# Performance work log

Measured on AMD Instinct MI355X. Metric: run time of the kernel, lower is better.

## Reference

```python
import jax, jax.numpy as jnp
import numpy as np

# Config (matches init_kwargs + Mamba2 defaults: expand=2, headdim=64, ngroups=1)
B_, C_IN, T, H, W = 4, 23, 8, 128, 128
P = 4
DM = 256
D_STATE = 16
D_CONV = 4
EXPAND = 2
D_INNER = EXPAND * DM            # 512
HEADDIM = 64
NHEADS = D_INNER // HEADDIM      # 8
CONV_DIM = D_INNER + 2 * D_STATE # 544 (ngroups=1)
D_IN_PROJ = 2 * D_INNER + 2 * D_STATE + NHEADS


def setup_inputs() -> dict:
    key = jax.random.key(0)
    ks = jax.random.split(key, 12)
    s = lambda k, shape, sc: (jax.random.normal(k, shape, jnp.float32) * sc)
    x = jax.random.normal(ks[0], (B_, C_IN, T, H, W), jnp.float32)
    patch_w = s(ks[1], (DM, C_IN, P, P), 0.05)       # Conv3d weight, depth-1 dim squeezed
    patch_b = s(ks[2], (DM,), 0.02)
    W_in = s(ks[3], (DM, D_IN_PROJ), 0.05)           # in_proj (bias=False)
    conv_w = s(ks[4], (CONV_DIM, D_CONV), 0.2)       # depthwise conv1d weight
    conv_b = s(ks[5], (CONV_DIM,), 0.02)
    dt_bias = jnp.log(jnp.expm1(jnp.exp(jax.random.uniform(ks[6], (NHEADS,), jnp.float32, jnp.log(1e-3), jnp.log(1e-1)))))
    A_log = jnp.log(jnp.arange(1, NHEADS + 1, dtype=jnp.float32))
    D_param = jnp.ones((NHEADS,), jnp.float32)
    norm_w = jnp.ones((D_INNER,), jnp.float32)
    W_out = s(ks[7], (D_INNER, DM), 0.05)            # out_proj (bias=False)
    unembed_w = s(ks[8], (DM, C_IN, P, P), 0.05)     # ConvTranspose3d weight (in,out,1,p,p)
    unembed_b = s(ks[9], (C_IN,), 0.02)
    return {"x": x, "patch_w": patch_w, "patch_b": patch_b, "W_in": W_in,
            "conv_w": conv_w, "conv_b": conv_b, "dt_bias": dt_bias, "A_log": A_log,
            "D_param": D_param, "norm_w": norm_w, "W_out": W_out,
            "unembed_w": unembed_w, "unembed_b": unembed_b}


def reference(x, patch_w, patch_b, W_in, conv_w, conv_b, dt_bias, A_log,
              D_param, norm_w, W_out, unembed_w, unembed_b):
    B, C, Tt, Hh, Ww = x.shape
    p = patch_w.shape[-1]
    Hp, Wp = Hh // p, Ww // p
    L = Tt * Hp * Wp
    # --- Conv3d patch embed (kernel (1,p,p), stride (1,p,p)) == non-overlapping patchify ---
    xr = x.reshape(B, C, Tt, Hp, p, Wp, p)
    emb = jnp.einsum('bcthiwj,dcij->bthwd', xr, patch_w) + patch_b  # [B,T,Hp,Wp,D]
    xs = emb.reshape(B, L, DM)
    # --- Mamba2 ---
    zxbcdt = xs @ W_in                                 # [B,L,2*d_inner+2*d_state+nheads]
    z = zxbcdt[:, :, :D_INNER]
    xBC = zxbcdt[:, :, D_INNER:D_INNER + CONV_DIM]
    dt = zxbcdt[:, :, D_INNER + CONV_DIM:]             # [B,L,nheads]
    # causal depthwise conv1d + silu
    xp = jnp.pad(xBC, ((0, 0), (D_CONV - 1, 0), (0, 0)))
    conv_out = conv_b + sum(xp[:, k:k + L, :] * conv_w[:, k] for k in range(D_CONV))
    xBC = jax.nn.silu(conv_out)
    xh = xBC[:, :, :D_INNER].reshape(B, L, NHEADS, HEADDIM)
    Bm = xBC[:, :, D_INNER:D_INNER + D_STATE]          # [B,L,N] (ngroups=1)
    Cm = xBC[:, :, D_INNER + D_STATE:]                 # [B,L,N]
    dt = jax.nn.softplus(dt + dt_bias)                 # [B,L,H]
    A = -jnp.exp(A_log)                                # [H]
    dA = jnp.exp(dt * A)                               # [B,L,H]
    xdt = xh * dt[..., None]                           # [B,L,H,P]
    # selective state-space scan: h_t = dA_t h_{t-1} + (dt_t x_t) B_t^T ; y_t = h_t C_t
    def step(h, inp):
        dA_t, xdt_t, B_t, C_t = inp
        h = dA_t[..., None, None] * h + jnp.einsum('bhp,bn->bhpn', xdt_t, B_t)
        y = jnp.einsum('bhpn,bn->bhp', h, C_t)
        return h, y
    inps = (dA.transpose(1, 0, 2), xdt.transpose(1, 0, 2, 3),
            Bm.transpose(1, 0, 2), Cm.transpose(1, 0, 2))
    h0 = jnp.zeros((B, NHEADS, HEADDIM, D_STATE), xs.dtype)
    _, ys = jax.lax.scan(step, h0, inps)               # [L,B,H,P]
    y = ys.transpose(1, 0, 2, 3) + D_param[None, None, :, None] * xh
    y = y.reshape(B, L, D_INNER)
    # gated RMSNorm (norm_before_gate=False): rmsnorm(y * silu(z)) * w
    yg = y * jax.nn.silu(z)
    y = yg * jax.lax.rsqrt(jnp.mean(yg * yg, axis=-1, keepdims=True) + 1e-5) * norm_w
    out_seq = y @ W_out                                # [B,L,DM]
    # --- ConvTranspose3d unembed (kernel (1,p,p), stride (1,p,p)) == un-patchify ---
    outp = out_seq.reshape(B, Tt, Hp, Wp, DM)
    un = jnp.einsum('bthwd,dcij->bcthiwj', outp, unembed_w)
    out = un.reshape(B, C, Tt, Hh, Ww) + unembed_b[None, :, None, None, None]
    return out + x
```

## Files before the change

kernel.cpp:

```cpp
#include <hip/hip_runtime.h>
#include <hip/hip_bf16.h>
#include <cstdint>
#include <cstddef>

#define B_N       4
#define C_INCH    23
#define T_N       8
#define W_IMG     128
#define L_SEQ     8192
#define BLROWS    32768
#define DM_       256
#define D_INNER_  512
#define CONV_DIM_ 544
#define D_PROJ    1064
#define KPATCH    368
#define QCH       64
#define NCH       128
#define RECW      56
#define PFD       8

typedef unsigned short ushort_t;
typedef unsigned int uint_t;
typedef __attribute__((ext_vector_type(8))) short short8;
typedef __attribute__((ext_vector_type(4))) float f32x4;

__device__ __forceinline__ float b2f(ushort_t u) {
    union { float f; uint_t u; } v; v.u = ((uint_t)u) << 16; return v.f;
}
__device__ __forceinline__ ushort_t f2b(float f) {
    union { float f; uint_t u; } v; v.f = f;
    uint_t r = v.u + 0x7fffu + ((v.u >> 16) & 1u);
    return (ushort_t)(r >> 16);
}

__device__ __forceinline__ void gload_lds16(const ushort_t* g, ushort_t* l) {
    __builtin_amdgcn_global_load_lds(
        (const __attribute__((address_space(1))) unsigned int*)g,
        (__attribute__((address_space(3))) unsigned int*)l, 16, 0, 0);
}

__device__ __forceinline__ short8 frag8(const float* q, bool live) {
    short8 f;
    if (live) {
        float4 lo = *(const float4*)q, hi = *(const float4*)(q + 4);
        f[0] = (short)f2b(lo.x); f[1] = (short)f2b(lo.y);
        f[2] = (short)f2b(lo.z); f[3] = (short)f2b(lo.w);
        f[4] = (short)f2b(hi.x); f[5] = (short)f2b(hi.y);
        f[6] = (short)f2b(hi.z); f[7] = (short)f2b(hi.w);
    } else {
        #pragma unroll
        for (int e = 0; e < 8; ++e) f[e] = 0;
    }
    return f;
}

__global__ void k_transcast(const float* __restrict__ src, ushort_t* __restrict__ dst,
                            int K, int N, const float* __restrict__ rscale) {
    int n = blockIdx.x;
    for (int k = threadIdx.x; k < K; k += 256) {
        float v = 0.f;
        if (n < N) {
            v = src[(size_t)k * N + n];
            if (rscale) v *= rscale[k];
        }
        dst[(size_t)n * K + k] = f2b(v);
    }
}

__global__ void k_castpad(const float* __restrict__ src, ushort_t* __restrict__ dst) {
    int d = blockIdx.x; int k = threadIdx.x;
    dst[d * 384 + k] = (k < KPATCH) ? f2b(src[d * KPATCH + k]) : (ushort_t)0;
}

__global__ void __launch_bounds__(256) k_pgemm(const float* __restrict__ x,
                                               const ushort_t* __restrict__ Wt,
                                               ushort_t* __restrict__ Cv,
                                               const float* __restrict__ bias) {
    __shared__ ushort_t Al[128 * 64];
    __shared__ ushort_t Bl[128 * 64];
    const int tid = threadIdx.x;
    const int w = tid >> 6, lane = tid & 63;
    const int wr = w >> 1, wc = w & 1;
    const int rowbase = blockIdx.y * 128;
    const int colbase = blockIdx.x * 128;
    const int g = lane >> 4, r = lane & 15;
    const int b  = rowbase >> 13;
    const int t  = (rowbase >> 10) & 7;
    const int hp0 = (rowbase >> 5) & 31;

    f32x4 acc[4][4];
    #pragma unroll
    for (int i = 0; i < 4; ++i)
        #pragma unroll
        for (int j = 0; j < 4; ++j) acc[i][j] = (f32x4){0.f, 0.f, 0.f, 0.f};

    for (int it = 0; it < 6; ++it) {
        int k0 = it * 64;
        __syncthreads();
        #pragma unroll
        for (int i2 = 0; i2 < 4; ++i2) {
            int s = i2 * 256 + (w << 6) + lane;
            int row = s >> 3;
            int c16 = (s & 7) ^ (row & 7);
            gload_lds16(Wt + (size_t)(colbase + row) * 384 + k0 + c16 * 8,
                        &Bl[(size_t)(i2 * 256 + (w << 6)) * 8]);
        }
        #pragma unroll
        for (int i2 = 0; i2 < 8; ++i2) {
            int idx = i2 * 256 + tid;
            int row = idx >> 4, kq = idx & 15;
            int c = (k0 >> 4) + (kq >> 2);
            int i = kq & 3;
            uint_t u0 = 0, u1 = 0;
            if (c < C_INCH) {
                int hp = hp0 + (row >> 5), wp = row & 31;
                const float4 v = *(const float4*)&x[(((size_t)(b * C_INCH + c) * T_N + t) << 14)
                                                    + (size_t)(hp * 4 + i) * W_IMG + wp * 4];
                u0 = (uint_t)f2b(v.x) | ((uint_t)f2b(v.y) << 16);
                u1 = (uint_t)f2b(v.z) | ((uint_t)f2b(v.w) << 16);
            }
            int slot = (row << 3) + ((kq >> 1) ^ (row & 7));
            *(uint2*)&Al[(size_t)slot * 8 + (kq & 1) * 4] = make_uint2(u0, u1);
        }
        __syncthreads();

        short8 af[2][4], bf[2][4];
        #pragma unroll
        for (int ks = 0; ks < 2; ++ks)
            #pragma unroll
            for (int mi = 0; mi < 4; ++mi) {
                int row = (wr << 6) + (mi << 4) + r;
                int c16 = ((ks << 2) | g) ^ (row & 7);
                af[ks][mi] = *(const short8*)&Al[(size_t)((row << 3) + c16) * 8];
            }
        #pragma unroll
        for (int ks = 0; ks < 2; ++ks)
            #pragma unroll
            for (int ni = 0; ni < 4; ++ni) {
                int row = (wc << 6) + (ni << 4) + r;
                int c16 = ((ks << 2) | g) ^ (row & 7);
                bf[ks][ni] = *(const short8*)&Bl[(size_t)((row << 3) + c16) * 8];
            }
        #pragma unroll
        for (int ks = 0; ks < 2; ++ks)
            #pragma unroll
            for (int mi = 0; mi < 4; ++mi)
                #pragma unroll
                for (int ni = 0; ni < 4; ++ni)
                    acc[mi][ni] = __builtin_amdgcn_mfma_f32_16x16x32_bf16(
                        af[ks][mi], bf[ks][ni], acc[mi][ni], 0, 0, 0);
    }

    #pragma unroll
    for (int mi = 0; mi < 4; ++mi) {
        int rw = rowbase + (wr << 6) + (mi << 4) + (g << 2);
        #pragma unroll
        for (int ni = 0; ni < 4; ++ni) {
            int col = colbase + (wc << 6) + (ni << 4) + r;
            float bv = bias[col];
            f32x4 v = acc[mi][ni];
            #pragma unroll
            for (int j = 0; j < 4; ++j)
                Cv[(size_t)(rw + j) * DM_ + col] = f2b(v[j] + bv);
        }
    }
}

template <int K, int N, bool CBF, bool ASCALE>
__global__ void __launch_bounds__(256) k_mgemm(const ushort_t* __restrict__ A, const int lda,
                                               const ushort_t* __restrict__ Wt,
                                               void* __restrict__ Cv, const int ldc, const int coff,
                                               const float* __restrict__ bias) {
    __shared__ ushort_t Al[128 * 64];
    __shared__ ushort_t Bl[128 * 64];
    const int tid = threadIdx.x;
    const int w = tid >> 6, lane = tid & 63;
    const int wr = w >> 1, wc = w & 1;
    const int rowbase = blockIdx.y * 128;
    const int colbase = blockIdx.x * 128;
    const int g = lane >> 4, r = lane & 15;

    f32x4 acc[4][4];
    #pragma unroll
    for (int i = 0; i < 4; ++i)
        #pragma unroll
        for (int j = 0; j < 4; ++j) acc[i][j] = (f32x4){0.f, 0.f, 0.f, 0.f};
    float rs[4] = {0.f, 0.f, 0.f, 0.f};

    for (int k0 = 0; k0 < K; k0 += 64) {
        __syncthreads();
        #pragma unroll
        for (int it = 0; it < 4; ++it) {
            int s = it * 256 + (w << 6) + lane;
            int row = s >> 3;
            int c16 = (s & 7) ^ (row & 7);
            gload_lds16(A + (size_t)(rowbase + row) * lda + k0 + c16 * 8,
                        &Al[(size_t)(it * 256 + (w << 6)) * 8]);
        }
        #pragma unroll
        for (int it = 0; it < 4; ++it) {
            int s = it * 256 + (w << 6) + lane;
            int row = s >> 3;
            int c16 = (s & 7) ^ (row & 7);
            gload_lds16(Wt + (size_t)(colbase + row) * K + k0 + c16 * 8,
                        &Bl[(size_t)(it * 256 + (w << 6)) * 8]);
        }
        __syncthreads();

        short8 af[2][4], bf[2][4];
        #pragma unroll
        for (int ks = 0; ks < 2; ++ks)
            #pragma unroll
            for (int mi = 0; mi < 4; ++mi) {
                int row = (wr << 6) + (mi << 4) + r;
                int c16 = ((ks << 2) | g) ^ (row & 7);
                af[ks][mi] = *(const short8*)&Al[(size_t)((row << 3) + c16) * 8];
            }
        #pragma unroll
        for (int ks = 0; ks < 2; ++ks)
            #pragma unroll
            for (int ni = 0; ni < 4; ++ni) {
                int row = (wc << 6) + (ni << 4) + r;
                int c16 = ((ks << 2) | g) ^ (row & 7);
                bf[ks][ni] = *(const short8*)&Bl[(size_t)((row << 3) + c16) * 8];
            }
        if (ASCALE) {
            #pragma unroll
            for (int ks = 0; ks < 2; ++ks)
                #pragma unroll
                for (int mi = 0; mi < 4; ++mi)
                    #pragma unroll
                    for (int e = 0; e < 8; ++e) {
                        float v = b2f((ushort_t)af[ks][mi][e]);
                        rs[mi] += v * v;
                    }
        }
        #pragma unroll
        for (int ks = 0; ks < 2; ++ks)
            #pragma unroll
            for (int mi = 0; mi < 4; ++mi)
                #pragma unroll
                for (int ni = 0; ni < 4; ++ni)
                    acc[mi][ni] = __builtin_amdgcn_mfma_f32_16x16x32_bf16(
                        af[ks][mi], bf[ks][ni], acc[mi][ni], 0, 0, 0);
    }

    #pragma unroll
    for (int mi = 0; mi < 4; ++mi) {
        int rw = rowbase + (wr << 6) + (mi << 4) + (g << 2);
        float sj[4] = {1.f, 1.f, 1.f, 1.f};
        if (ASCALE) {
            float s = rs[mi];
            s += __shfl_xor(s, 16);
            s += __shfl_xor(s, 32);
            float sc = rsqrtf(s * (1.f / 512.f) + 1e-5f);
            #pragma unroll
            for (int j = 0; j < 4; ++j) sj[j] = __shfl(sc, 4 * g + j);
        }
        #pragma unroll
        for (int ni = 0; ni < 4; ++ni) {
            int col = colbase + (wc << 6) + (ni << 4) + r;
            if (col < N) {
                float bv = bias ? bias[col] : 0.f;
                f32x4 v = acc[mi][ni];
                #pragma unroll
                for (int j = 0; j < 4; ++j) {
                    size_t cidx = (size_t)(rw + j) * ldc + coff + col;
                    float vr = v[j] * sj[j] + bv;
                    if (CBF) ((ushort_t*)Cv)[cidx] = f2b(vr);
                    else     ((float*)Cv)[cidx]   = vr;
                }
            }
        }
    }
}

__global__ void __launch_bounds__(256) k_conv(const ushort_t* __restrict__ xbcdt,
                                              const float* __restrict__ cw,
                                              const float* __restrict__ cb,
                                              const float* __restrict__ dtb,
                                              const float* __restrict__ alog,
                                              ushort_t* __restrict__ xbc,
                                              float* __restrict__ brec) {
    int tid = threadIdx.x;
    int rb = blockIdx.x * 8;
    int srb = rb & (L_SEQ - 1);
    #pragma unroll
    for (int it = 0; it < 3; ++it) {
        int ch = it * 256 + tid;
        if (ch >= 552) break;
        if (ch < CONV_DIM_) {
            float w0 = cw[ch * 4 + 0], w1 = cw[ch * 4 + 1];
            float w2 = cw[ch * 4 + 2], w3 = cw[ch * 4 + 3];
            float bias = cb[ch];
            float win[11];
            #pragma unroll
            for (int j = 0; j < 11; ++j) {
                int sj = srb + j - 3;
                win[j] = (sj >= 0) ? b2f(xbcdt[(size_t)(rb + j - 3) * 640 + ch]) : 0.f;
            }
            #pragma unroll
            for (int r = 0; r < 8; ++r) {
                float acc = bias + win[r] * w0 + win[r + 1] * w1 + win[r + 2] * w2 + win[r + 3] * w3;
                float s = acc / (1.f + __expf(-acc));
                size_t row = rb + r;
                if (ch < 512) xbc[row * 512 + ch] = f2b(s);
                else          brec[row * RECW + (ch - 512)] = s;
            }
        } else {
            int h = ch - CONV_DIM_;
            float A = -__expf(alog[h]);
            float db = dtb[h];
            #pragma unroll
            for (int r = 0; r < 8; ++r) {
                size_t row = rb + r;
                float v = b2f(xbcdt[row * 640 + ch]) + db;
                float sp = (v > 20.f) ? v : log1pf(__expf(v));
                brec[row * RECW + 32 + h] = __expf(sp * A);
                brec[row * RECW + 40 + h] = sp;
                brec[row * RECW + 48 + h] = sp * A;
            }
        }
    }
}

__global__ void __launch_bounds__(256) k_scan1(const ushort_t* __restrict__ xbc,
                                               const float* __restrict__ brec,
                                               float* __restrict__ sbuf,
                                               float* __restrict__ cdf) {
    __shared__ float rec[QCH * RECW];
    int c = blockIdx.x, b = blockIdx.z;
    int tid = threadIdx.x;
    int h = blockIdx.y * 4 + (tid >> 6);
    int p = tid & 63;
    int off = h * 64 + p;
    size_t row0 = (size_t)b * L_SEQ + (size_t)c * QCH;

    {
        const float4* src = (const float4*)(brec + row0 * RECW);
        float4* dst = (float4*)rec;
        #pragma unroll
        for (int i = 0; i < 3; ++i) dst[i * 256 + tid] = src[i * 256 + tid];
        if (tid < 128) dst[768 + tid] = src[768 + tid];
    }

    float st[16];
    #pragma unroll
    for (int n = 0; n < 16; ++n) st[n] = 0.f;
    float cd = 1.f;
    float xh[PFD];
    #pragma unroll
    for (int j = 0; j < PFD; ++j) xh[j] = b2f(xbc[(row0 + j) * 512 + off]);
    __syncthreads();

    for (int s0 = 0; s0 < QCH; s0 += PFD) {
        float xhn[PFD];
        #pragma unroll
        for (int j = 0; j < PFD; ++j)
            xhn[j] = b2f(xbc[(row0 + s0 + PFD + j) * 512 + off]);
        #pragma unroll
        for (int j = 0; j < PFD; ++j) {
            const float* r = rec + (s0 + j) * RECW;
            float da  = r[32 + h];
            float dtt = r[40 + h];
            float xdt = xh[j] * dtt;
            const float4* B4 = (const float4*)r;
            #pragma unroll
            for (int q = 0; q < 4; ++q) {
                float4 Bv = B4[q];
                st[q*4+0] = da * st[q*4+0] + xdt * Bv.x;
                st[q*4+1] = da * st[q*4+1] + xdt * Bv.y;
                st[q*4+2] = da * st[q*4+2] + xdt * Bv.z;
                st[q*4+3] = da * st[q*4+3] + xdt * Bv.w;
            }
            cd *= da;
        }
        #pragma unroll
        for (int j = 0; j < PFD; ++j) xh[j] = xhn[j];
    }
    size_t base = (size_t)((b * 8 + h) * NCH + c) * 1024 + p * 16;
    #pragma unroll
    for (int q = 0; q < 4; ++q)
        *(float4*)&sbuf[base + q * 4] = make_float4(st[q*4], st[q*4+1], st[q*4+2], st[q*4+3]);
    if (p == 0) cdf[(b * 8 + h) * NCH + c] = cd;
}

__global__ void __launch_bounds__(256) k_chain(const float* __restrict__ sbuf,
                                               const float* __restrict__ cdf,
                                               float* __restrict__ hin) {
    int h = blockIdx.x, b = blockIdx.y;
    int tid = threadIdx.x;
    float4 H = make_float4(0.f, 0.f, 0.f, 0.f);
    size_t base = (size_t)((b * 8 + h) * NCH) * 1024;
    for (int c = 0; c < NCH; ++c) {
        *(float4*)&hin[base + (size_t)c * 1024 + tid * 4] = H;
        float cdfv = cdf[(b * 8 + h) * NCH + c];
        float4 S = *(const float4*)&sbuf[base + (size_t)c * 1024 + tid * 4];
        H.x = cdfv * H.x + S.x;
        H.y = cdfv * H.y + S.y;
        H.z = cdfv * H.z + S.z;
        H.w = cdfv * H.w + S.w;
    }
}

__global__ void __launch_bounds__(64) k_ssc2(const ushort_t* __restrict__ xbc,
                                             const ushort_t* __restrict__ z_bf,
                                             const float* __restrict__ brec,
                                             const float* __restrict__ Dp,
                                             const float* __restrict__ hin,
                                             ushort_t* __restrict__ yg_out) {
    __shared__ ushort_t XhT[64 * 72];
    __shared__ ushort_t Pl [64 * 72];
    __shared__ float Sl[64], Tl[64], El[64];
    const int c = blockIdx.x, h = blockIdx.y, b = blockIdx.z;
    const int lane = threadIdx.x;
    const int g = lane >> 4, r = lane & 15;
    const size_t row0 = (size_t)b * L_SEQ + (size_t)c * QCH;
    const size_t bhc = (size_t)(b * 8 + h) * NCH + c;

    uint4 xw[8];
    {
        const uint4* xsrc = (const uint4*)(xbc + (row0 + lane) * 512 + h * 64);
        #pragma unroll
        for (int q = 0; q < 8; ++q) xw[q] = xsrc[q];
    }
    float ldA = brec[(row0 + lane) * RECW + 48 + h];
    float dtv = brec[(row0 + lane) * RECW + 40 + h];

    float S = ldA;
    #pragma unroll
    for (int d = 1; d < 64; d <<= 1) {
        float o = __shfl(S, (lane >= d) ? (lane - d) : 0);
        if (lane >= d) S += o;
    }
    Sl[lane] = S;
    Tl[lane] = S - __logf(dtv);
    El[lane] = __expf(S);

    #pragma unroll
    for (int p = 0; p < 64; ++p) {
        uint4 v = xw[p >> 3];
        int sub = (p >> 1) & 3;
        uint_t word = (sub == 0) ? v.x : (sub == 1) ? v.y : (sub == 2) ? v.z : v.w;
        XhT[p * 72 + lane] = (ushort_t)((p & 1) ? (word >> 16) : (word & 0xffffu));
    }

    short8 cwf[4], bwf[4];
    #pragma unroll
    for (int t4 = 0; t4 < 4; ++t4) {
        cwf[t4] = frag8(brec + (row0 + t4 * 16 + r) * RECW + 16 + g * 8, g < 2);
        bwf[t4] = frag8(brec + (row0 + t4 * 16 + r) * RECW + 0  + g * 8, g < 2);
    }
    __syncthreads();

    #pragma unroll
    for (int j0t = 0; j0t < 4; ++j0t) {
        #pragma unroll
        for (int i0t = 0; i0t < 4; ++i0t) {
            f32x4 m = (f32x4){0.f, 0.f, 0.f, 0.f};
            m = __builtin_amdgcn_mfma_f32_16x16x32_bf16(bwf[j0t], cwf[i0t], m, 0, 0, 0);
            int i = i0t * 16 + r;
            float si = Sl[i];
            float4 tj = *(const float4*)&Tl[j0t * 16 + g * 4];
            ushort_t pv[4];
            #pragma unroll
            for (int reg = 0; reg < 4; ++reg) {
                int j = j0t * 16 + g * 4 + reg;
                float tjv = (reg == 0) ? tj.x : (reg == 1) ? tj.y : (reg == 2) ? tj.z : tj.w;
                float mask = (j <= i) ? __expf(si - tjv) : 0.f;
                pv[reg] = f2b(m[reg] * mask);
            }
            uint2 packed = make_uint2((uint_t)pv[0] | ((uint_t)pv[1] << 16),
                                      (uint_t)pv[2] | ((uint_t)pv[3] << 16));
            *(uint2*)&Pl[i * 72 + j0t * 16 + g * 4] = packed;
        }
    }
    __syncthreads();

    short8 xhf[4][2];
    #pragma unroll
    for (int p0t = 0; p0t < 4; ++p0t)
        #pragma unroll
        for (int kk = 0; kk < 2; ++kk)
            xhf[p0t][kk] = *(const short8*)&XhT[(p0t * 16 + r) * 72 + kk * 32 + g * 8];
    short8 hinf[4];
    #pragma unroll
    for (int p0t = 0; p0t < 4; ++p0t)
        hinf[p0t] = frag8(hin + bhc * 1024 + (size_t)(p0t * 16 + r) * 16 + g * 8, g < 2);

    const float Dh = Dp[h];

    #pragma unroll
    for (int i0t = 0; i0t < 4; ++i0t) {
        short8 pa0 = *(const short8*)&Pl[(i0t * 16 + r) * 72 + 0  + g * 8];
        short8 pa1 = *(const short8*)&Pl[(i0t * 16 + r) * 72 + 32 + g * 8];
        float4 e4 = *(const float4*)&El[i0t * 16 + g * 4];
        #pragma unroll
        for (int p0t = 0; p0t < 4; ++p0t) {
            f32x4 acc = (f32x4){0.f, 0.f, 0.f, 0.f};
            acc = __builtin_amdgcn_mfma_f32_16x16x32_bf16(cwf[i0t], hinf[p0t], acc, 0, 0, 0);
            acc[0] *= e4.x; acc[1] *= e4.y; acc[2] *= e4.z; acc[3] *= e4.w;
            acc = __builtin_amdgcn_mfma_f32_16x16x32_bf16(pa0, xhf[p0t][0], acc, 0, 0, 0);
            acc = __builtin_amdgcn_mfma_f32_16x16x32_bf16(pa1, xhf[p0t][1], acc, 0, 0, 0);
            int p = p0t * 16 + r;
            #pragma unroll
            for (int reg = 0; reg < 4; ++reg) {
                int i = i0t * 16 + g * 4 + reg;
                size_t row = row0 + i;
                float xhv = b2f(XhT[p * 72 + i]);
                float y = acc[reg] + Dh * xhv;
                float zz = b2f(z_bf[row * 512 + h * 64 + p]);
                float ygv = y * (zz / (1.f + __expf(-zz)));
                yg_out[row * 512 + h * 64 + p] = f2b(ygv);
            }
        }
    }
}

__global__ void __launch_bounds__(256) k_scatter(const ushort_t* __restrict__ tmp,
                                                 const float* __restrict__ ub,
                                                 const float* __restrict__ xin,
                                                 float* __restrict__ out) {
    int tid = threadIdx.x;
    int w = tid & 127;
    int h = (blockIdx.x << 1) | (tid >> 7);
    int c = blockIdx.y >> 3, t = blockIdx.y & 7;
    int b = blockIdx.z;
    size_t row = (size_t)b * L_SEQ + t * 1024 + (h >> 2) * 32 + (w >> 2);
    int kk = c * 16 + (h & 3) * 4 + (w & 3);
    size_t oidx = (((size_t)(b * C_INCH + c) * T_N + t) << 14) + (size_t)h * W_IMG + w;
    out[oidx] = b2f(tmp[row * KPATCH + kk]) + ub[c] + xin[oidx];
}

extern "C" void kernel_launch(void* const* d_in, const int* in_sizes, int n_in,
                              void* d_out, int out_size, void* d_ws, size_t ws_size,
                              hipStream_t stream) {
    const float* x       = (const float*)d_in[0];
    const float* patch_w = (const float*)d_in[1];
    const float* patch_b = (const float*)d_in[2];
    const float* W_in    = (const float*)d_in[3];
    const float* conv_w  = (const float*)d_in[4];
    const float* conv_b  = (const float*)d_in[5];
    const float* dt_bias = (const float*)d_in[6];
    const float* A_log   = (const float*)d_in[7];
    const float* D_param = (const float*)d_in[8];
    const float* norm_w  = (const float*)d_in[9];
    const float* W_out   = (const float*)d_in[10];
    const float* unemb_w = (const float*)d_in[11];
    const float* unemb_b = (const float*)d_in[12];
    float* out = (float*)d_out;

    char* p = (char*)d_ws;
    ushort_t* scratch = (ushort_t*)p; p += (size_t)BLROWS * 384 * 2;
    float* cdf  = (float*)p;   p += (size_t)32 * NCH * 4;
    float* sbuf = (float*)p;   p += (size_t)32 * NCH * 1024 * 4;
    float* hin  = (float*)p;   p += (size_t)32 * NCH * 1024 * 4;
    float* brec = (float*)p;   p += (size_t)BLROWS * RECW * 4;
    ushort_t* Wt_p   = (ushort_t*)p; p += (size_t)256 * 384 * 2;
    ushort_t* Wt_in  = (ushort_t*)p; p += (size_t)1152 * 256 * 2;
    ushort_t* Wt_out = (ushort_t*)p; p += (size_t)256 * 512 * 2;
    ushort_t* Wt_un  = (ushort_t*)p; p += (size_t)384 * 256 * 2;
    ushort_t* xs     = (ushort_t*)p; p += (size_t)BLROWS * DM_ * 2;
    ushort_t* xbc    = (ushort_t*)p; p += (size_t)BLROWS * 512 * 2;
    ushort_t* z_bf   = (ushort_t*)p; p += (size_t)BLROWS * 512 * 2;
    ushort_t* xbcdt  = (ushort_t*)p; p += (size_t)BLROWS * 640 * 2;
    size_t need = (size_t)(p - (char*)d_ws);
    if (ws_size < need) return;

    ushort_t* tmp = scratch;
    ushort_t* yg  = xbcdt;

    k_castpad<<<256, 384, 0, stream>>>(patch_w, Wt_p);
    k_transcast<<<1152, 256, 0, stream>>>(W_in, Wt_in, 256, 1064, nullptr);
    k_transcast<<<256, 256, 0, stream>>>(W_out, Wt_out, 512, 256, norm_w);
    k_transcast<<<384, 256, 0, stream>>>(unemb_w, Wt_un, 256, 368, nullptr);

    k_pgemm<<<dim3(2, 256), 256, 0, stream>>>(x, Wt_p, xs, patch_b);

    k_mgemm<256, 512, true, false><<<dim3(4, 256), 256, 0, stream>>>(xs, 256, Wt_in, z_bf, 512, 0, nullptr);
    k_mgemm<256, 552, true, false><<<dim3(5, 256), 256, 0, stream>>>(xs, 256, Wt_in + (size_t)512 * 256, xbcdt, 640, 0, nullptr);

    k_conv<<<BLROWS / 8, 256, 0, stream>>>(xbcdt, conv_w, conv_b, dt_bias, A_log, xbc, brec);

    k_scan1<<<dim3(NCH, 2, 4), 256, 0, stream>>>(xbc, brec, sbuf, cdf);
    k_chain<<<dim3(8, 4), 256, 0, stream>>>(sbuf, cdf, hin);
    k_ssc2<<<dim3(NCH, 8, 4), 64, 0, stream>>>(xbc, z_bf, brec, D_param, hin, yg);

    k_mgemm<512, 256, true, true><<<dim3(2, 256), 256, 0, stream>>>(yg, 512, Wt_out, xs, DM_, 0, nullptr);

    k_mgemm<256, 368, true, false><<<dim3(3, 256), 256, 0, stream>>>(xs, 256, Wt_un, tmp, KPATCH, 0, nullptr);

    k_scatter<<<dim3(64, 184, 4), 256, 0, stream>>>(tmp, unemb_b, x, out);
}
```

Before: 256.6 us.

## Compute chunk end-states with MFMA instead of sequential scan; stage B/C via LDS

Replaces the per-chunk sequential recurrence in k_scan1 with a closed-form chunk state: prefix-sum the log decay, weight B rows by dt*exp(Stot - S_j), and form the state as an Xh^T x Bw matrix product on bf16 MFMA. The launch becomes one 64-thread wave per (chunk, head, batch). k_ssc2 also stages B/C into LDS as bf16 through coalesced loads instead of per-lane fragment gathers. This removes the serial 64-step dependency chain but adds bf16 rounding to the state and weights.

```diff
diff --git a/kernel.cpp b/kernel.cpp
--- a/kernel.cpp
+++ b/kernel.cpp
@@ -17,7 +17,6 @@
 #define QCH       64
 #define NCH       128
 #define RECW      56
-#define PFD       8
 
 typedef unsigned short ushort_t;
 typedef unsigned int uint_t;
@@ -324,65 +323,83 @@
     }
 }
 
-__global__ void __launch_bounds__(256) k_scan1(const ushort_t* __restrict__ xbc,
+__global__ void __launch_bounds__(64) k_scan1m(const ushort_t* __restrict__ xbc,
                                                const float* __restrict__ brec,
                                                float* __restrict__ sbuf,
                                                float* __restrict__ cdf) {
-    __shared__ float rec[QCH * RECW];
-    int c = blockIdx.x, b = blockIdx.z;
-    int tid = threadIdx.x;
-    int h = blockIdx.y * 4 + (tid >> 6);
-    int p = tid & 63;
-    int off = h * 64 + p;
-    size_t row0 = (size_t)b * L_SEQ + (size_t)c * QCH;
-
+    __shared__ ushort_t XhT[64 * 72];
+    __shared__ float    Bst[64 * 20];
+    __shared__ ushort_t BwT[16 * 72];
+    const int c = blockIdx.x, h = blockIdx.y, b = blockIdx.z;
+    const int lane = threadIdx.x;
+    const int g = lane >> 4, r = lane & 15;
+    const size_t row0 = (size_t)b * L_SEQ + (size_t)c * QCH;
+
+    uint4 xw[8];
     {
-        const float4* src = (const float4*)(brec + row0 * RECW);
-        float4* dst = (float4*)rec;
-        #pragma unroll
-        for (int i = 0; i < 3; ++i) dst[i * 256 + tid] = src[i * 256 + tid];
-        if (tid < 128) dst[768 + tid] = src[768 + tid];
-    }
-
-    float st[16];
-    #pragma unroll
-    for (int n = 0; n < 16; ++n) st[n] = 0.f;
-    float cd = 1.f;
-    float xh[PFD];
-    #pragma unroll
-    for (int j = 0; j < PFD; ++j) xh[j] = b2f(xbc[(row0 + j) * 512 + off]);
+        const uint4* xsrc = (const uint4*)(xbc + (row0 + lane) * 512 + h * 64);
+        #pragma unroll
+        for (int q = 0; q < 8; ++q) xw[q] = xsrc[q];
+    }
+    #pragma unroll
+    for (int it2 = 0; it2 < 4; ++it2) {
+        int idx = it2 * 64 + lane;
+        int row = idx >> 2, q = idx & 3;
+        float4 v = *(const float4*)(brec + (row0 + row) * RECW + q * 4);
+        *(float4*)&Bst[row * 20 + q * 4] = v;
+    }
+    float ldA = brec[(row0 + lane) * RECW + 48 + h];
+    float dtv = brec[(row0 + lane) * RECW + 40 + h];
+
+    float S = ldA;
+    #pragma unroll
+    for (int d = 1; d < 64; d <<= 1) {
+        float o = __shfl(S, (lane >= d) ? (lane - d) : 0);
+        if (lane >= d) S += o;
+    }
+    float Stot = __shfl(S, 63);
+    float wj = dtv * __expf(Stot - S);
+
+    #pragma unroll
+    for (int p = 0; p < 64; ++p) {
+        uint4 v = xw[p >> 3];
+        int sub = (p >> 1) & 3;
+        uint_t word = (sub == 0) ? v.x : (sub == 1) ? v.y : (sub == 2) ? v.z : v.w;
+        XhT[p * 72 + lane] = (ushort_t)((p & 1) ? (word >> 16) : (word & 0xffffu));
+    }
     __syncthreads();
 
-    for (int s0 = 0; s0 < QCH; s0 += PFD) {
-        float xhn[PFD];
-        #pragma unroll
-        for (int j = 0; j < PFD; ++j)
-            xhn[j] = b2f(xbc[(row0 + s0 + PFD + j) * 512 + off]);
-        #pragma unroll
-        for (int j = 0; j < PFD; ++j) {
-            const float* r = rec + (s0 + j) * RECW;
-            float da  = r[32 + h];
-            float dtt = r[40 + h];
-            float xdt = xh[j] * dtt;
-            const float4* B4 = (const float4*)r;
-            #pragma unroll
-            for (int q = 0; q < 4; ++q) {
-                float4 Bv = B4[q];
-                st[q*4+0] = da * st[q*4+0] + xdt * Bv.x;
-                st[q*4+1] = da * st[q*4+1] + xdt * Bv.y;
-                st[q*4+2] = da * st[q*4+2] + xdt * Bv.z;
-                st[q*4+3] = da * st[q*4+3] + xdt * Bv.w;
-            }
-            cd *= da;
-        }
-        #pragma unroll
-        for (int j = 0; j < PFD; ++j) xh[j] = xhn[j];
-    }
-    size_t base = (size_t)((b * 8 + h) * NCH + c) * 1024 + p * 16;
-    #pragma unroll
-    for (int q = 0; q < 4; ++q)
-        *(float4*)&sbuf[base + q * 4] = make_float4(st[q*4], st[q*4+1], st[q*4+2], st[q*4+3]);
-    if (p == 0) cdf[(b * 8 + h) * NCH + c] = cd;
+    {
+        const float* bp = &Bst[lane * 20];
+        float4 b0 = *(const float4*)bp;
+        float4 b1 = *(const float4*)(bp + 4);
+        float4 b2 = *(const float4*)(bp + 8);
+        float4 b3 = *(const float4*)(bp + 12);
+        float bv[16] = {b0.x,b0.y,b0.z,b0.w, b1.x,b1.y,b1.z,b1.w,
+                        b2.x,b2.y,b2.z,b2.w, b3.x,b3.y,b3.z,b3.w};
+        #pragma unroll
+        for (int n = 0; n < 16; ++n)
+            BwT[n * 72 + lane] = f2b(bv[n] * wj);
+    }
+    __syncthreads();
+
+    short8 bwtf[2];
+    bwtf[0] = *(const short8*)&BwT[r * 72 + 0  + g * 8];
+    bwtf[1] = *(const short8*)&BwT[r * 72 + 32 + g * 8];
+
+    size_t base = ((size_t)(b * 8 + h) * NCH + c) * 1024;
+    #pragma unroll
+    for (int p0t = 0; p0t < 4; ++p0t) {
+        short8 a0 = *(const short8*)&XhT[(p0t * 16 + r) * 72 + 0  + g * 8];
+        short8 a1 = *(const short8*)&XhT[(p0t * 16 + r) * 72 + 32 + g * 8];
+        f32x4 acc = (f32x4){0.f, 0.f, 0.f, 0.f};
+        acc = __builtin_amdgcn_mfma_f32_16x16x32_bf16(a0, bwtf[0], acc, 0, 0, 0);
+        acc = __builtin_amdgcn_mfma_f32_16x16x32_bf16(a1, bwtf[1], acc, 0, 0, 0);
+        #pragma unroll
+        for (int reg = 0; reg < 4; ++reg)
+            sbuf[base + (size_t)(p0t * 16 + g * 4 + reg) * 16 + r] = acc[reg];
+    }
+    if (lane == 63) cdf[(b * 8 + h) * NCH + c] = __expf(S);
 }
 
 __global__ void __launch_bounds__(256) k_chain(const float* __restrict__ sbuf,
@@ -424,6 +441,15 @@
         #pragma unroll
         for (int q = 0; q < 8; ++q) xw[q] = xsrc[q];
     }
+    #pragma unroll
+    for (int it2 = 0; it2 < 8; ++it2) {
+        int idx = it2 * 64 + lane;
+        int row = idx >> 3, q = idx & 7;
+        float4 v = *(const float4*)(brec + (row0 + row) * RECW + q * 4);
+        uint_t u0 = (uint_t)f2b(v.x) | ((uint_t)f2b(v.y) << 16);
+        uint_t u1 = (uint_t)f2b(v.z) | ((uint_t)f2b(v.w) << 16);
+        *(uint2*)&Pl[row * 40 + q * 4] = make_uint2(u0, u1);
+    }
     float ldA = brec[(row0 + lane) * RECW + 48 + h];
     float dtv = brec[(row0 + lane) * RECW + 40 + h];
 
@@ -444,12 +470,18 @@
         uint_t word = (sub == 0) ? v.x : (sub == 1) ? v.y : (sub == 2) ? v.z : v.w;
         XhT[p * 72 + lane] = (ushort_t)((p & 1) ? (word >> 16) : (word & 0xffffu));
     }
+    __syncthreads();
 
     short8 cwf[4], bwf[4];
     #pragma unroll
     for (int t4 = 0; t4 < 4; ++t4) {
-        cwf[t4] = frag8(brec + (row0 + t4 * 16 + r) * RECW + 16 + g * 8, g < 2);
-        bwf[t4] = frag8(brec + (row0 + t4 * 16 + r) * RECW + 0  + g * 8, g < 2);
+        if (g < 2) {
+            bwf[t4] = *(const short8*)&Pl[(t4 * 16 + r) * 40 + 0  + g * 8];
+            cwf[t4] = *(const short8*)&Pl[(t4 * 16 + r) * 40 + 16 + g * 8];
+        } else {
+            #pragma unroll
+            for (int e = 0; e < 8; ++e) { bwf[t4][e] = 0; cwf[t4][e] = 0; }
+        }
     }
     __syncthreads();
 
@@ -582,7 +614,7 @@
 
     k_conv<<<BLROWS / 8, 256, 0, stream>>>(xbcdt, conv_w, conv_b, dt_bias, A_log, xbc, brec);
 
-    k_scan1<<<dim3(NCH, 2, 4), 256, 0, stream>>>(xbc, brec, sbuf, cdf);
+    k_scan1m<<<dim3(NCH, 8, 4), 64, 0, stream>>>(xbc, brec, sbuf, cdf);
     k_chain<<<dim3(8, 4), 256, 0, stream>>>(sbuf, cdf, hin);
     k_ssc2<<<dim3(NCH, 8, 4), 64, 0, stream>>>(xbc, z_bf, brec, D_param, hin, yg);
 
```

Measured after the change: 250.3 us. 1.03x faster.
